# Performance work log

Measured on AMD Instinct MI355X. Metric: run time of the kernel, lower is better.

The kernel has to match this reference:

```python
import jax, jax.numpy as jnp
import numpy as np

DEPTH = 4
CH = 3
SIG_CHANNELS = 3 + 9 + 27 + 81  # signatory.signature_channels(3, 4) = 120


def _tp(a, b):
    # flattened tensor (outer) product: (N, p) x (N, q) -> (N, p*q), row-major (signatory ordering)
    return (a[:, :, None] * b[:, None, :]).reshape(a.shape[0], -1)


def _signature(path):
    """Depth-4 path signature of path: (N, T, 3) -> (N, 120).

    Segment signature of a linear piece with increment dx is exp(dx):
    levels dx^{otimes k} / k!. Segments are combined with Chen's identity
    via a lax.scan over the time axis.
    """
    dx = path[:, 1:, :] - path[:, :-1, :]  # (N, T-1, 3)
    N, Tm1, _ = dx.shape
    dt = path.dtype
    # per-segment signature levels (flattened)
    s1 = dx                                                                # (N,T-1,3)
    s2 = (s1[..., :, None] * dx[..., None, :]).reshape(N, Tm1, 9) / 2.0   # dx^2/2!
    s3 = (s2[..., :, None] * dx[..., None, :]).reshape(N, Tm1, 27) / 3.0  # dx^3/3!
    s4 = (s3[..., :, None] * dx[..., None, :]).reshape(N, Tm1, 81) / 4.0  # dx^4/4!
    segs = (jnp.moveaxis(s1, 1, 0), jnp.moveaxis(s2, 1, 0),
            jnp.moveaxis(s3, 1, 0), jnp.moveaxis(s4, 1, 0))  # time-leading for scan

    init = (jnp.zeros((N, 3), dt), jnp.zeros((N, 9), dt),
            jnp.zeros((N, 27), dt), jnp.zeros((N, 81), dt))

    def chen_step(carry, seg):
        c1, c2, c3, c4 = carry
        g1, g2, g3, g4 = seg
        n1 = c1 + g1
        n2 = c2 + _tp(c1, g1) + g2
        n3 = c3 + _tp(c2, g1) + _tp(c1, g2) + g3
        n4 = c4 + _tp(c3, g1) + _tp(c2, g2) + _tp(c1, g3) + g4
        return (n1, n2, n3, n4), None

    (c1, c2, c3, c4), _ = jax.lax.scan(chen_step, init, segs)
    return jnp.concatenate([c1, c2, c3, c4], axis=1)  # (N, 120)


def setup_inputs() -> dict:
    key = jax.random.key(0)
    k1, k2, k3, k4, k5 = jax.random.split(key, 5)
    B, T, V, M = 64, 300, 17, 2
    inp = jax.random.normal(k1, (B, CH, T, V, M), dtype=jnp.float32)
    fan1 = 34 * SIG_CHANNELS  # 4080
    W1 = jax.random.uniform(k2, (512, fan1), jnp.float32, -1.0, 1.0) / np.sqrt(fan1)
    b1 = jax.random.uniform(k3, (512,), jnp.float32, -1.0, 1.0) / np.sqrt(fan1)
    W2 = jax.random.uniform(k4, (155, 512), jnp.float32, -1.0, 1.0) / np.sqrt(512)
    b2 = jax.random.uniform(k5, (155,), jnp.float32, -1.0, 1.0) / np.sqrt(512)
    return {"inp": inp, "W1": W1, "b1": b1, "W2": W2, "b2": b2}


def reference(inp, W1, b1, W2, b2):
    B, _, T, V, M = inp.shape
    # order matches the torch loop: for v in range(17): for m in range(2)
    paths = jnp.transpose(inp, (0, 3, 4, 2, 1)).reshape(B * V * M, T, CH)  # (B*34, T, 3)
    sig = _signature(paths).reshape(B, V * M * SIG_CHANNELS)  # (B, 4080)
    h = sig @ W1.T + b1  # dropout is identity in eval mode
    return h @ W2.T + b2  # (B, 155)
```

## Files before the change

kernel.cpp:

```cpp
#include <hip/hip_runtime.h>
#include <hip/hip_bf16.h>

#define B_SZ 64
#define T_PTS 300
#define N_SEG 299
#define VM 34
#define NPATH (B_SZ*VM)
#define SIGC 120
#define FAN1 4080
#define H1 512
#define NOUT 155
#define GSZ 16
#define CHUNK 19
#define TT 75
#define KSPL 48
#define KW 85

__device__ __forceinline__ void sig_append(float a1[3], float a2[9], float a3[27], float a4[81],
                                           float d0, float d1, float d2) {
  float B1[3] = {d0, d1, d2};
  float Hh[3] = {0.5f * d0, 0.5f * d1, 0.5f * d2};
  float Tt[3] = {(1.0f / 3.0f) * d0, (1.0f / 3.0f) * d1, (1.0f / 3.0f) * d2};
  float Qq[3] = {0.25f * d0, 0.25f * d1, 0.25f * d2};
  float B2[9], B3[27];
#pragma unroll
  for (int i = 0; i < 3; i++)
#pragma unroll
    for (int j = 0; j < 3; j++) B2[i * 3 + j] = B1[i] * Hh[j];
#pragma unroll
  for (int e = 0; e < 27; e++) B3[e] = B2[e / 3] * Tt[e % 3];

#pragma unroll
  for (int e = 0; e < 81; e++) {
    float v = a4[e];
    v = fmaf(B3[e / 3], Qq[e % 3], v);
    v = fmaf(a3[e / 3], B1[e % 3], v);
    v = fmaf(a2[e / 9], B2[e % 9], v);
    v = fmaf(a1[e / 27], B3[e % 27], v);
    a4[e] = v;
  }
#pragma unroll
  for (int e = 0; e < 27; e++) {
    float v = a3[e] + B3[e];
    v = fmaf(a2[e / 3], B1[e % 3], v);
    v = fmaf(a1[e / 9], B2[e % 9], v);
    a3[e] = v;
  }
#pragma unroll
  for (int e = 0; e < 9; e++) a2[e] = fmaf(a1[e / 3], B1[e % 3], a2[e] + B2[e]);
  a1[0] += d0; a1[1] += d1; a1[2] += d2;
}

__global__ __launch_bounds__(256) void transpose_kernel(const float* __restrict__ inp,
                                                        float* __restrict__ tp,
                                                        const float* __restrict__ b1,
                                                        float* __restrict__ ht) {
  const int b = blockIdx.x;
  const int tile = blockIdx.y;
  const int t0 = tile * TT;
  const int tid = threadIdx.x;
  __shared__ float lds[3 * TT * VM];

  const float* src = inp + (size_t)b * 3 * T_PTS * VM;
  for (int idx = tid; idx < 3 * TT * VM; idx += 256) {
    const int c = idx / (TT * VM);
    const int rem = idx - c * (TT * VM);
    lds[idx] = src[(c * T_PTS + t0) * VM + rem];
  }
  __syncthreads();

  for (int idx = tid; idx < VM * TT * 3; idx += 256) {
    const int vm = idx / (TT * 3);
    const int i = idx - vm * (TT * 3);
    const int tt = i / 3;
    const int c = i - tt * 3;
    tp[((size_t)(b * VM + vm) * T_PTS + t0 + tt) * 3 + c] = lds[(c * TT + tt) * VM + vm];
  }

  if (tile == 0) {
    for (int idx = tid; idx < 8 * 64; idx += 256)
      ht[(size_t)(8 * b) * 64 + idx] = b1[8 * b + (idx >> 6)];
  }
}

__global__ __launch_bounds__(64)
__attribute__((amdgpu_waves_per_eu(1)))
void sig_kernel(const float* __restrict__ tp, float* __restrict__ St) {
  const int lane = threadIdx.x & 63;
  const int g = lane >> 4;
  const int sub = lane & (GSZ - 1);
  const int p = blockIdx.x * 4 + g;
  const int t0 = sub * CHUNK;

  const float* bp = tp + (size_t)p * (T_PTS * 3) + t0 * 3;

  float a1[3], a2[9], a3[27], a4[81];
#pragma unroll
  for (int i = 0; i < 3; i++) a1[i] = 0.f;
#pragma unroll
  for (int i = 0; i < 9; i++) a2[i] = 0.f;
#pragma unroll
  for (int i = 0; i < 27; i++) a3[i] = 0.f;
#pragma unroll
  for (int i = 0; i < 81; i++) a4[i] = 0.f;

  float x0 = bp[0], x1 = bp[1], x2 = bp[2];
  for (int s = 0; s < CHUNK; s++) {
    const float y0 = bp[3 * s + 3];
    const float y1 = bp[3 * s + 4];
    const float y2 = bp[3 * s + 5];
    const bool valid = (t0 + s) < N_SEG;
    const float d0 = valid ? (y0 - x0) : 0.0f;
    const float d1 = valid ? (y1 - x1) : 0.0f;
    const float d2 = valid ? (y2 - x2) : 0.0f;
    sig_append(a1, a2, a3, a4, d0, d1, d2);
    x0 = y0; x1 = y1; x2 = y2;
  }

#pragma unroll
  for (int off = 1; off < GSZ; off <<= 1) {
    const float m = (sub + off < GSZ) ? 1.0f : 0.0f;
    float B1[3], B2[9], B3[27];
#pragma unroll
    for (int i = 0; i < 3; i++) B1[i] = m * __shfl_down(a1[i], off);
#pragma unroll
    for (int i = 0; i < 9; i++) B2[i] = m * __shfl_down(a2[i], off);
#pragma unroll
    for (int i = 0; i < 27; i++) B3[i] = m * __shfl_down(a3[i], off);

#pragma unroll
    for (int e = 0; e < 81; e++) {
      const float b4 = m * __shfl_down(a4[e], off);
      float v = a4[e] + b4;
      v = fmaf(a3[e / 3], B1[e % 3], v);
      v = fmaf(a2[e / 9], B2[e % 9], v);
      v = fmaf(a1[e / 27], B3[e % 27], v);
      a4[e] = v;
    }
#pragma unroll
    for (int e = 0; e < 27; e++) {
      float v = a3[e] + B3[e];
      v = fmaf(a2[e / 3], B1[e % 3], v);
      v = fmaf(a1[e / 9], B2[e % 9], v);
      a3[e] = v;
    }
#pragma unroll
    for (int e = 0; e < 9; e++) a2[e] = fmaf(a1[e / 3], B1[e % 3], a2[e] + B2[e]);
#pragma unroll
    for (int i = 0; i < 3; i++) a1[i] += B1[i];
  }

  if (sub == 0) {
    const int b = p / VM;
    const int vm = p - b * VM;
    float* dst = St + (size_t)(vm * SIGC) * 64 + b;
#pragma unroll
    for (int i = 0; i < 3; i++) dst[(size_t)i * 64] = a1[i];
#pragma unroll
    for (int i = 0; i < 9; i++) dst[(size_t)(3 + i) * 64] = a2[i];
#pragma unroll
    for (int i = 0; i < 27; i++) dst[(size_t)(12 + i) * 64] = a3[i];
#pragma unroll
    for (int i = 0; i < 81; i++) dst[(size_t)(39 + i) * 64] = a4[i];
  }
}

__global__ __launch_bounds__(256) void gemm1_kernel(const float* __restrict__ St,
                                                    const float* __restrict__ W1,
                                                    float* __restrict__ ht) {
  const int lane = threadIdx.x & 63;
  int wave_id = (blockIdx.x * 256 + threadIdx.x) >> 6;
  wave_id = __builtin_amdgcn_readfirstlane(wave_id);
  const int ks = wave_id / 128;
  const int jg = wave_id & 127;
  const int k0 = ks * KW;

  const float* stp = St + (size_t)k0 * 64 + lane;
  const float* w0 = W1 + (size_t)(jg * 4 + 0) * FAN1 + k0;
  const float* w1 = W1 + (size_t)(jg * 4 + 1) * FAN1 + k0;
  const float* w2 = W1 + (size_t)(jg * 4 + 2) * FAN1 + k0;
  const float* w3 = W1 + (size_t)(jg * 4 + 3) * FAN1 + k0;

  float sv[KW];
#pragma unroll
  for (int i = 0; i < KW; i++) sv[i] = stp[(size_t)i * 64];

  float acc0 = 0.f, acc1 = 0.f, acc2 = 0.f, acc3 = 0.f;
#pragma unroll
  for (int i = 0; i < KW; i++) {
    acc0 = fmaf(sv[i], w0[i], acc0);
    acc1 = fmaf(sv[i], w1[i], acc1);
    acc2 = fmaf(sv[i], w2[i], acc2);
    acc3 = fmaf(sv[i], w3[i], acc3);
  }

  float* hp = ht + (size_t)(jg * 4) * 64 + lane;
  atomicAdd(hp + 0 * 64, acc0);
  atomicAdd(hp + 1 * 64, acc1);
  atomicAdd(hp + 2 * 64, acc2);
  atomicAdd(hp + 3 * 64, acc3);
}

__global__ __launch_bounds__(256) void gemm2_kernel(const float* __restrict__ ht,
                                                    const float* __restrict__ W2,
                                                    const float* __restrict__ b2,
                                                    float* __restrict__ out) {
  const int j = blockIdx.x;
  const int lane = threadIdx.x & 63;
  int w = threadIdx.x >> 6;
  w = __builtin_amdgcn_readfirstlane(w);
  __shared__ float red[4][64];

  const float* htp = ht + (size_t)(w * 128) * 64 + lane;
  const float* w2r = W2 + (size_t)j * H1 + w * 128;
  float acc = 0.f;
#pragma unroll 8
  for (int k = 0; k < 128; k++) acc = fmaf(w2r[k], htp[(size_t)k * 64], acc);

  red[w][lane] = acc;
  __syncthreads();
  if (threadIdx.x < 64) {
    const float tot = red[0][lane] + red[1][lane] + red[2][lane] + red[3][lane];
    out[(size_t)lane * NOUT + j] = tot + b2[j];
  }
}

extern "C" void kernel_launch(void* const* d_in, const int* in_sizes, int n_in,
                              void* d_out, int out_size, void* d_ws, size_t ws_size,
                              hipStream_t stream) {
  const float* inp = (const float*)d_in[0];
  const float* W1  = (const float*)d_in[1];
  const float* b1  = (const float*)d_in[2];
  const float* W2  = (const float*)d_in[3];
  const float* b2  = (const float*)d_in[4];
  float* out = (float*)d_out;

  float* tpbuf = (float*)d_ws;
  float* St    = tpbuf + (size_t)NPATH * T_PTS * 3;
  float* ht    = St + (size_t)FAN1 * 64;

  transpose_kernel<<<dim3(B_SZ, 4), 256, 0, stream>>>(inp, tpbuf, b1, ht);
  sig_kernel<<<NPATH / 4, 64, 0, stream>>>(tpbuf, St);
  gemm1_kernel<<<KSPL * 128 / 4, 256, 0, stream>>>(St, W1, ht);
  gemm2_kernel<<<NOUT, 256, 0, stream>>>(ht, W2, b2, out);
}
```

Before: 120.9 us.

## Map one path per wave with 64-lane Chen tree using DPP shifts

The signature kernel now gives each path a full 64-lane wave instead of 16 lanes. Each lane handles 5 segments instead of 19, and the partial signatures are then merged by a 6-round Chen tree reduction. Offsets below 16 use DPP row-shift moves instead of ds_bpermute shuffles, and the per-round validity mask is dropped because out-of-row lanes read zero. The aim is to shorten the serial per-lane segment chain, at the cost of four times as many waves and two extra reduction rounds.

```diff
diff --git a/kernel.cpp b/kernel.cpp
--- a/kernel.cpp
+++ b/kernel.cpp
@@ -10,8 +10,7 @@
 #define FAN1 4080
 #define H1 512
 #define NOUT 155
-#define GSZ 16
-#define CHUNK 19
+#define CHUNK 5
 #define TT 75
 #define KSPL 48
 #define KW 85
@@ -49,6 +48,48 @@
 #pragma unroll
   for (int e = 0; e < 9; e++) a2[e] = fmaf(a1[e / 3], B1[e % 3], a2[e] + B2[e]);
   a1[0] += d0; a1[1] += d1; a1[2] += d2;
+}
+
+template <int OFF>
+__device__ __forceinline__ float lane_down(float x) {
+  if constexpr (OFF < 16) {
+    return __int_as_float(__builtin_amdgcn_update_dpp(
+        0, __float_as_int(x), 0x100 + OFF , 0xF, 0xF, true));
+  } else {
+    return __shfl_xor(x, OFF);
+  }
+}
+
+template <int OFF>
+__device__ __forceinline__ void chen_round(float a1[3], float a2[9], float a3[27], float a4[81]) {
+  float B1[3], B2[9], B3[27];
+#pragma unroll
+  for (int i = 0; i < 3; i++) B1[i] = lane_down<OFF>(a1[i]);
+#pragma unroll
+  for (int i = 0; i < 9; i++) B2[i] = lane_down<OFF>(a2[i]);
+#pragma unroll
+  for (int i = 0; i < 27; i++) B3[i] = lane_down<OFF>(a3[i]);
+
+#pragma unroll
+  for (int e = 0; e < 81; e++) {
+    const float b4 = lane_down<OFF>(a4[e]);
+    float v = a4[e] + b4;
+    v = fmaf(a3[e / 3], B1[e % 3], v);
+    v = fmaf(a2[e / 9], B2[e % 9], v);
+    v = fmaf(a1[e / 27], B3[e % 27], v);
+    a4[e] = v;
+  }
+#pragma unroll
+  for (int e = 0; e < 27; e++) {
+    float v = a3[e] + B3[e];
+    v = fmaf(a2[e / 3], B1[e % 3], v);
+    v = fmaf(a1[e / 9], B2[e % 9], v);
+    a3[e] = v;
+  }
+#pragma unroll
+  for (int e = 0; e < 9; e++) a2[e] = fmaf(a1[e / 3], B1[e % 3], a2[e] + B2[e]);
+#pragma unroll
+  for (int i = 0; i < 3; i++) a1[i] += B1[i];
 }
 
 __global__ __launch_bounds__(256) void transpose_kernel(const float* __restrict__ inp,
@@ -87,10 +128,8 @@
 __attribute__((amdgpu_waves_per_eu(1)))
 void sig_kernel(const float* __restrict__ tp, float* __restrict__ St) {
   const int lane = threadIdx.x & 63;
-  const int g = lane >> 4;
-  const int sub = lane & (GSZ - 1);
-  const int p = blockIdx.x * 4 + g;
-  const int t0 = sub * CHUNK;
+  const int p = blockIdx.x;
+  const int t0 = lane * CHUNK;
 
   const float* bp = tp + (size_t)p * (T_PTS * 3) + t0 * 3;
 
@@ -105,6 +144,7 @@
   for (int i = 0; i < 81; i++) a4[i] = 0.f;
 
   float x0 = bp[0], x1 = bp[1], x2 = bp[2];
+#pragma unroll
   for (int s = 0; s < CHUNK; s++) {
     const float y0 = bp[3 * s + 3];
     const float y1 = bp[3 * s + 4];
@@ -117,40 +157,14 @@
     x0 = y0; x1 = y1; x2 = y2;
   }
 
-#pragma unroll
-  for (int off = 1; off < GSZ; off <<= 1) {
-    const float m = (sub + off < GSZ) ? 1.0f : 0.0f;
-    float B1[3], B2[9], B3[27];
-#pragma unroll
-    for (int i = 0; i < 3; i++) B1[i] = m * __shfl_down(a1[i], off);
-#pragma unroll
-    for (int i = 0; i < 9; i++) B2[i] = m * __shfl_down(a2[i], off);
-#pragma unroll
-    for (int i = 0; i < 27; i++) B3[i] = m * __shfl_down(a3[i], off);
-
-#pragma unroll
-    for (int e = 0; e < 81; e++) {
-      const float b4 = m * __shfl_down(a4[e], off);
-      float v = a4[e] + b4;
-      v = fmaf(a3[e / 3], B1[e % 3], v);
-      v = fmaf(a2[e / 9], B2[e % 9], v);
-      v = fmaf(a1[e / 27], B3[e % 27], v);
-      a4[e] = v;
-    }
-#pragma unroll
-    for (int e = 0; e < 27; e++) {
-      float v = a3[e] + B3[e];
-      v = fmaf(a2[e / 3], B1[e % 3], v);
-      v = fmaf(a1[e / 9], B2[e % 9], v);
-      a3[e] = v;
-    }
-#pragma unroll
-    for (int e = 0; e < 9; e++) a2[e] = fmaf(a1[e / 3], B1[e % 3], a2[e] + B2[e]);
-#pragma unroll
-    for (int i = 0; i < 3; i++) a1[i] += B1[i];
-  }
-
-  if (sub == 0) {
+  chen_round<1>(a1, a2, a3, a4);
+  chen_round<2>(a1, a2, a3, a4);
+  chen_round<4>(a1, a2, a3, a4);
+  chen_round<8>(a1, a2, a3, a4);
+  chen_round<16>(a1, a2, a3, a4);
+  chen_round<32>(a1, a2, a3, a4);
+
+  if (lane == 0) {
     const int b = p / VM;
     const int vm = p - b * VM;
     float* dst = St + (size_t)(vm * SIGC) * 64 + b;
@@ -240,7 +254,7 @@
   float* ht    = St + (size_t)FAN1 * 64;
 
   transpose_kernel<<<dim3(B_SZ, 4), 256, 0, stream>>>(inp, tpbuf, b1, ht);
-  sig_kernel<<<NPATH / 4, 64, 0, stream>>>(tpbuf, St);
+  sig_kernel<<<NPATH, 64, 0, stream>>>(tpbuf, St);
   gemm1_kernel<<<KSPL * 128 / 4, 256, 0, stream>>>(St, W1, ht);
   gemm2_kernel<<<NOUT, 256, 0, stream>>>(ht, W2, b2, out);
 }
```

Result: no change. 119.0 us (-1.5%).
